# Kernel optimization log

Measured on AMD Instinct MI355X. Metric: run time of the kernel, lower is better.

Reference implementation:

```python
import jax, jax.numpy as jnp
import numpy as np

H = 256; NL = 6; N = 64; DCONV = 4; DIN = 512; HEADS = 8; P = 64
CONVD = DIN + 2 * N            # 640
PROJ = 2 * DIN + 2 * N + HEADS  # 1160


def rmsnorm(x, w, eps=1e-6):
    return x * jax.lax.rsqrt(jnp.mean(x * x, axis=-1, keepdims=True) + eps) * w


def mamba2(x, Win, conv_w, conv_b, dt_bias, A_log, D, gnorm, Wout):
    # x: (b, l, H)
    b, l, _ = x.shape
    zxbcdt = x @ Win                       # (b, l, PROJ)
    z = zxbcdt[..., :DIN]
    xBC = zxbcdt[..., DIN:DIN + CONVD]
    dt = zxbcdt[..., DIN + CONVD:]         # (b, l, HEADS)
    # causal depthwise conv1d along l
    xp = jnp.pad(xBC, ((0, 0), (DCONV - 1, 0), (0, 0)))
    xc = conv_b + sum(xp[:, k:k + l, :] * conv_w[k] for k in range(DCONV))
    xBC = jax.nn.silu(xc)
    xs = xBC[..., :DIN]
    B = xBC[..., DIN:DIN + N]
    C = xBC[..., DIN + N:]
    dt = jax.nn.softplus(dt + dt_bias)
    dA = jnp.exp(dt * (-jnp.exp(A_log)))   # (b, l, HEADS)
    xh = xs.reshape(b, l, HEADS, P)
    xdt = xh * dt[..., None]

    def step(h, inp):
        dA_t, xdt_t, B_t, C_t = inp
        h = dA_t[:, :, None, None] * h + xdt_t[..., None] * B_t[:, None, None, :]
        return h, jnp.einsum('bhpn,bn->bhp', h, C_t)

    h0 = jnp.zeros((b, HEADS, P, N), x.dtype)
    _, ys = jax.lax.scan(step, h0, (jnp.swapaxes(dA, 0, 1), jnp.swapaxes(xdt, 0, 1),
                                    jnp.swapaxes(B, 0, 1), jnp.swapaxes(C, 0, 1)))
    y = jnp.swapaxes(ys, 0, 1) + D[None, None, :, None] * xh   # (b, l, HEADS, P)
    y = y.reshape(b, l, DIN) * jax.nn.silu(z)
    return rmsnorm(y, gnorm) @ Wout


def dual_path(x, t_norm, t_Win, t_cw, t_cb, t_dtb, t_Alog, t_D, t_gn, t_Wout,
              b_norm, b_Win, b_cw, b_cb, b_dtb, b_Alog, b_D, b_gn, b_Wout):
    batch, time, bands, hdim = x.shape
    for i in range(NL):
        # time-axis pass (raw row-major reshape, matching torch .reshape semantics)
        xt = x.reshape(batch * bands, time, hdim)
        xt = xt + mamba2(rmsnorm(xt, t_norm[i]), t_Win[i], t_cw[i], t_cb[i],
                         t_dtb[i], t_Alog[i], t_D[i], t_gn[i], t_Wout[i])
        x = jnp.swapaxes(xt.reshape(batch, bands, time, hdim), 1, 2)
        # band-axis pass
        xb = x.reshape(batch * time, bands, hdim)
        xb = xb + mamba2(rmsnorm(xb, b_norm[i]), b_Win[i], b_cw[i], b_cb[i],
                         b_dtb[i], b_Alog[i], b_D[i], b_gn[i], b_Wout[i])
        x = xb.reshape(batch, time, bands, hdim)
    return x


def setup_inputs() -> dict:
    key = jax.random.key(0)
    ks = jax.random.split(key, 3)
    x = jax.random.normal(ks[0], (2, 512, 64, H), jnp.float32)

    def make_params(k):
        kk = jax.random.split(k, 5)
        g = lambda kx, sh, s: jax.random.normal(kx, sh, jnp.float32) * s
        return dict(
            norm=jnp.ones((NL, H), jnp.float32),
            Win=g(kk[0], (NL, H, PROJ), H ** -0.5),
            cw=g(kk[1], (NL, DCONV, CONVD), 0.2),
            cb=jnp.zeros((NL, CONVD), jnp.float32),
            dtb=g(kk[2], (NL, HEADS), 0.5),
            Alog=jnp.log(jnp.abs(g(kk[3], (NL, HEADS), 1.0)) + 0.5),
            D=jnp.ones((NL, HEADS), jnp.float32),
            gn=jnp.ones((NL, DIN), jnp.float32),
            Wout=g(kk[4], (NL, DIN, H), DIN ** -0.5),
        )

    tp = make_params(ks[1]); bp = make_params(ks[2])
    out = {'x': x}
    for name, d in (('t', tp), ('b', bp)):
        for kname, v in d.items():
            out[f'{name}_{kname}'] = v
    return out


def reference(x, t_norm, t_Win, t_cw, t_cb, t_dtb, t_Alog, t_D, t_gn, t_Wout,
              b_norm, b_Win, b_cw, b_cb, b_dtb, b_Alog, b_D, b_gn, b_Wout):
    return dual_path(x, t_norm, t_Win, t_cw, t_cb, t_dtb, t_Alog, t_D, t_gn, t_Wout,
                     b_norm, b_Win, b_cw, b_cb, b_dtb, b_Alog, b_D, b_gn, b_Wout)
```

## Files before the change

kernel.cpp:

```cpp
#include <hip/hip_runtime.h>
#include <math.h>

#define NLAY   6
#define Hd     256
#define DINv   512
#define NHEADS 8
#define CONVDv 640
#define PROJv  1160
#define ZW     656
#define NTOK   65536
#define NCH    1024

typedef __attribute__((ext_vector_type(8))) short bf16x8;
typedef __attribute__((ext_vector_type(4))) float f32x4;
typedef unsigned short u16;

__device__ __forceinline__ float siluf(float v) {
    return v * __builtin_amdgcn_rcpf(1.0f + __expf(-v));
}
__device__ __forceinline__ float bflo(unsigned u) { return __uint_as_float(u << 16); }
__device__ __forceinline__ float bfhi(unsigned u) { return __uint_as_float(u & 0xffff0000u); }
__device__ __forceinline__ u16 f2b(float f) {
    unsigned u = __float_as_uint(f);
    return (u16)((u + 0x7fffu + ((u >> 16) & 1u)) >> 16);
}
__device__ __forceinline__ float b2f(u16 s) { return __uint_as_float(((unsigned)s) << 16); }

__device__ __forceinline__ void gl_lds16(const void* g, void* l) {
    __builtin_amdgcn_global_load_lds((const __attribute__((address_space(1))) unsigned int*)g,
                                     (__attribute__((address_space(3))) unsigned int*)l, 16, 0, 0);
}

__global__ __launch_bounds__(512)
void kprep_win(const float* __restrict__ tW, const float* __restrict__ bW,
               u16* __restrict__ Whi, u16* __restrict__ Wlo)
{
    const int li = blockIdx.y, j = blockIdx.x;
    const int t  = threadIdx.x;
    const int kk = t >> 6, col = (t >> 2) & 15, quad = t & 3;
    const float* W = (li < 6) ? (tW + (size_t)li * Hd * PROJv)
                              : (bW + (size_t)(li - 6) * Hd * PROJv);
    const int fullcol = 16 * j + col;
    const size_t ob = ((size_t)li * 74 + j) * 4096 + kk * 512 + quad * 128 + col * 8;
#pragma unroll
    for (int e = 0; e < 8; e++) {
        const int k = kk * 32 + quad * 8 + e;
        const float v = (fullcol < PROJv) ? W[(size_t)k * PROJv + fullcol] : 0.f;
        const u16 hi = f2b(v);
        Whi[ob + e] = hi;
        Wlo[ob + e] = f2b(v - b2f(hi));
    }
}

__global__ __launch_bounds__(512)
void kprep_wout(const float* __restrict__ tW, const float* __restrict__ tg,
                const float* __restrict__ bW, const float* __restrict__ bg,
                u16* __restrict__ Whi, u16* __restrict__ Wlo)
{
    const int li = blockIdx.y, j = blockIdx.x;
    const int t  = threadIdx.x;
    const int kk = t >> 5, col = (t >> 1) & 15, qh = t & 1;
    const float* W = (li < 6) ? tW + (size_t)li * DINv * Hd : bW + (size_t)(li - 6) * DINv * Hd;
    const float* g = (li < 6) ? tg + li * DINv : bg + (li - 6) * DINv;
    const int fullcol = 16 * j + col;
#pragma unroll
    for (int q = 0; q < 2; q++) {
        const int quad = qh * 2 + q;
        const size_t ob = ((size_t)li * 16 + j) * 8192 + kk * 512 + quad * 128 + col * 8;
#pragma unroll
        for (int e = 0; e < 8; e++) {
            const int k = kk * 32 + quad * 8 + e;
            const float v = W[(size_t)k * Hd + fullcol] * g[k];
            const u16 hi = f2b(v);
            Whi[ob + e] = hi;
            Wlo[ob + e] = f2b(v - b2f(hi));
        }
    }
}

__global__ __launch_bounds__(512, 4)
void k1_mfma(const float* __restrict__ src, u16* __restrict__ zs,
             u16* __restrict__ xrawT, u16* __restrict__ bnd,
             const float* __restrict__ nw,
             const u16* __restrict__ Whi, const u16* __restrict__ Wlo)
{
    __shared__ __align__(16) char smem[67584];
    u16* sAh = (u16*)smem;
    u16* sAl = sAh + 64 * 264;
    const int tid = threadIdx.x;
    const int cb  = blockIdx.x;
    const int R0  = cb * 64;

    {
        const int tok = tid >> 3, l8 = tid & 7;
        const float* xr = src + ((size_t)(R0 + tok)) * Hd + l8 * 32;
        float vv[32];
#pragma unroll
        for (int q = 0; q < 8; q++) {
            float4 v = ((const float4*)xr)[q];
            vv[4*q] = v.x; vv[4*q+1] = v.y; vv[4*q+2] = v.z; vv[4*q+3] = v.w;
        }
        float ss = 0.f;
#pragma unroll
        for (int j = 0; j < 32; j++) ss += vv[j] * vv[j];
#pragma unroll
        for (int m = 4; m >= 1; m >>= 1) ss += __shfl_xor(ss, m, 8);
        const float rstd = rsqrtf(ss * (1.0f / Hd) + 1e-6f);
        const float* nr = nw + l8 * 32;
        u16* dh = sAh + tok * 264 + l8 * 32;
        u16* dl = sAl + tok * 264 + l8 * 32;
#pragma unroll
        for (int j = 0; j < 32; j++) {
            const float val = vv[j] * rstd * nr[j];
            const u16 hi = f2b(val);
            dh[j] = hi;
            dl[j] = f2b(val - b2f(hi));
        }
    }
    __syncthreads();

    const int lane = tid & 63, wave = tid >> 6;
    const int rh = wave >> 1, cw = wave & 1;
    const int quad = lane >> 4, m16 = lane & 15;

    bf16x8 ah[8], al[8];
    {
        const u16* ph = sAh + (rh * 16 + m16) * 264 + quad * 8;
        const u16* pl = sAl + (rh * 16 + m16) * 264 + quad * 8;
#pragma unroll
        for (int kk = 0; kk < 8; kk++) {
            ah[kk] = *(const bf16x8*)(ph + kk * 32);
            al[kk] = *(const bf16x8*)(pl + kk * 32);
        }
    }
    __syncthreads();

    u16* sW = (u16*)smem;

#define K1_STAGE(p, buf)                                                          \
    {                                                                             \
        const int obase = wave * 4096;                                            \
        _Pragma("unroll")                                                         \
        for (int i = 0; i < 4; i++) {                                             \
            const int o = obase + i * 1024;                                       \
            const int chunk = o >> 13, t2 = chunk >> 1, hl = chunk & 1;           \
            const int within = o & 8191;                                          \
            const u16* sbase = (hl ? Wlo : Whi) + (size_t)(2 * (p) + t2) * 4096;  \
            gl_lds16((const char*)sbase + within + lane * 16,                     \
                     (char*)sW + (buf) * 32768 + o);                              \
        }                                                                         \
    }

    K1_STAGE(0, 0);
    __syncthreads();

    for (int p = 0; p < 37; p++) {
        if (p < 36) K1_STAGE(p + 1, (p + 1) & 1);
        const int j = 2 * p + cw;
        const u16* tb = sW + (p & 1) * 16384 + cw * 8192 + lane * 8;
        f32x4 acc = (f32x4){0.f, 0.f, 0.f, 0.f};
#pragma unroll
        for (int kk = 0; kk < 8; kk++) {
            bf16x8 bh = *(const bf16x8*)(tb + kk * 512);
            bf16x8 bl = *(const bf16x8*)(tb + 4096 + kk * 512);
            acc = __builtin_amdgcn_mfma_f32_16x16x32_bf16(ah[kk], bh, acc, 0, 0, 0);
            acc = __builtin_amdgcn_mfma_f32_16x16x32_bf16(al[kk], bh, acc, 0, 0, 0);
            acc = __builtin_amdgcn_mfma_f32_16x16x32_bf16(ah[kk], bl, acc, 0, 0, 0);
        }
        const int fullcol = 16 * j + m16;
        if (j < 32) {
            u16* zr = zs + (size_t)(R0 + rh * 16 + quad * 4) * ZW + fullcol;
#pragma unroll
            for (int i = 0; i < 4; i++) zr[(size_t)i * ZW] = f2b(acc[i]);
        } else if (j < 64) {
            const int ch = fullcol - 512;
            uint2 v;
            v.x = (unsigned)f2b(acc[0]) | ((unsigned)f2b(acc[1]) << 16);
            v.y = (unsigned)f2b(acc[2]) | ((unsigned)f2b(acc[3]) << 16);
            *(uint2*)(xrawT + ((size_t)cb * 512 + ch) * 64 + rh * 16 + quad * 4) = v;
            if (rh == 3 && quad == 3) {
#pragma unroll
                for (int i = 1; i < 4; i++)
                    bnd[((size_t)cb * 3 + (i - 1)) * 640 + ch] = f2b(acc[i]);
            }
        } else if (j < 73) {
            const int zc = fullcol - 512;
            u16* zr = zs + (size_t)(R0 + rh * 16 + quad * 4) * ZW + zc;
#pragma unroll
            for (int i = 0; i < 4; i++) zr[(size_t)i * ZW] = f2b(acc[i]);
            if (j < 72 && rh == 3 && quad == 3) {
#pragma unroll
                for (int i = 1; i < 4; i++)
                    bnd[((size_t)cb * 3 + (i - 1)) * 640 + zc] = f2b(acc[i]);
            }
        }
        __syncthreads();
    }
#undef K1_STAGE
}

__device__ __forceinline__ void conv32_rmw(u16* xp, float w0, float w1, float w2, float w3,
                                           float bias, float h3, float h2, float h1)
{
    uint4 va = ((const uint4*)xp)[0], vb = ((const uint4*)xp)[1],
          vc = ((const uint4*)xp)[2], vd = ((const uint4*)xp)[3];
    unsigned uu[16] = {va.x, va.y, va.z, va.w, vb.x, vb.y, vb.z, vb.w,
                       vc.x, vc.y, vc.z, vc.w, vd.x, vd.y, vd.z, vd.w};
    unsigned ou[16];
#pragma unroll
    for (int k = 0; k < 16; k++) {
        const float x0 = bflo(uu[k]);
        const u16 o0 = f2b(siluf(bias + w0*h3 + w1*h2 + w2*h1 + w3*x0));
        h3 = h2; h2 = h1; h1 = x0;
        const float x1 = bfhi(uu[k]);
        const u16 o1 = f2b(siluf(bias + w0*h3 + w1*h2 + w2*h1 + w3*x1));
        h3 = h2; h2 = h1; h1 = x1;
        ou[k] = (unsigned)o0 | ((unsigned)o1 << 16);
    }
    ((uint4*)xp)[0] = make_uint4(ou[0],  ou[1],  ou[2],  ou[3]);
    ((uint4*)xp)[1] = make_uint4(ou[4],  ou[5],  ou[6],  ou[7]);
    ((uint4*)xp)[2] = make_uint4(ou[8],  ou[9],  ou[10], ou[11]);
    ((uint4*)xp)[3] = make_uint4(ou[12], ou[13], ou[14], ou[15]);
}

__global__ __launch_bounds__(256, 4)
void k2a_conv(u16* __restrict__ zs, u16* __restrict__ xrawT,
              float* __restrict__ spb, const u16* __restrict__ bnd,
              const float* __restrict__ cwp, const float* __restrict__ cbp,
              const float* __restrict__ dtbp, const float* __restrict__ alogp, int L)
{
    __shared__ __align__(16) u16 sBC[64][128];
    const int tid = threadIdx.x;
    const int cb  = blockIdx.x;
    const size_t row0 = (size_t)cb * 64;
    const bool atStart = (((int)(row0 % (size_t)L)) == 0);
    const int lane = tid & 63, wave = tid >> 6;

#pragma unroll
    for (int j = 0; j < 4; j++) {
        const int t0 = wave * 16 + j * 4;
        gl_lds16(zs + (row0 + t0 + (lane >> 4)) * ZW + 512 + (lane & 15) * 8,
                 (char*)sBC + t0 * 256);
    }

#pragma unroll
    for (int cc = 0; cc < 2; cc++) {
        const int ch = tid + cc * 256;
        const float w0 = cwp[0*CONVDv + ch], w1 = cwp[1*CONVDv + ch],
                    w2 = cwp[2*CONVDv + ch], w3 = cwp[3*CONVDv + ch];
        u16* xp = xrawT + ((size_t)cb * 512 + ch) * 64 + 32;
        const uint2 hv = *(const uint2*)(xp - 4);
        conv32_rmw(xp, w0, w1, w2, w3, cbp[ch], bfhi(hv.x), bflo(hv.y), bfhi(hv.y));
    }

    if (tid < 64) {
        const int t = tid;
        const uint4 dv = *(const uint4*)(zs + (row0 + t) * ZW + 640);
        const unsigned uu[4] = {dv.x, dv.y, dv.z, dv.w};
        float sp[8], ld[8];
#pragma unroll
        for (int h = 0; h < 8; h++) {
            const float d = ((h & 1) ? bfhi(uu[h >> 1]) : bflo(uu[h >> 1])) + dtbp[h];
            const float s = (d > 20.f) ? d : __logf(1.f + __expf(d));
            sp[h] = s;
            ld[h] = -__expf(alogp[h]) * s;
        }
        float* ob = spb + (row0 + t) * 24;
        *(float4*)(ob)      = make_float4(sp[0], sp[1], sp[2], sp[3]);
        *(float4*)(ob + 4)  = make_float4(sp[4], sp[5], sp[6], sp[7]);
        *(float4*)(ob + 8)  = make_float4(ld[0], ld[1], ld[2], ld[3]);
        *(float4*)(ob + 12) = make_float4(ld[4], ld[5], ld[6], ld[7]);
    }
    __syncthreads();

#pragma unroll
    for (int cc = 0; cc < 2; cc++) {
        const int ch = tid + cc * 256;
        const float w0 = cwp[0*CONVDv + ch], w1 = cwp[1*CONVDv + ch],
                    w2 = cwp[2*CONVDv + ch], w3 = cwp[3*CONVDv + ch];
        float h1 = 0.f, h2 = 0.f, h3 = 0.f;
        if (!atStart) {
            const u16* bp = bnd + ((size_t)(cb - 1) * 3) * 640 + ch;
            h3 = b2f(bp[0]); h2 = b2f(bp[640]); h1 = b2f(bp[1280]);
        }
        conv32_rmw(xrawT + ((size_t)cb * 512 + ch) * 64, w0, w1, w2, w3, cbp[ch], h3, h2, h1);
    }

    u16 o[32];
    {
        const int ch  = tid & 127;
        const int th  = tid >> 7;
        const int t0  = th * 32;
        const int gch = 512 + ch;
        const float w0 = cwp[0*CONVDv + gch], w1 = cwp[1*CONVDv + gch],
                    w2 = cwp[2*CONVDv + gch], w3 = cwp[3*CONVDv + gch];
        const float bias = cbp[gch];
        float h1, h2, h3;
        if (th) {
            h3 = b2f(sBC[29][ch]); h2 = b2f(sBC[30][ch]); h1 = b2f(sBC[31][ch]);
        } else if (!atStart) {
            const u16* bp = bnd + ((size_t)(cb - 1) * 3) * 640 + gch;
            h3 = b2f(bp[0]); h2 = b2f(bp[640]); h1 = b2f(bp[1280]);
        } else { h1 = h2 = h3 = 0.f; }
#pragma unroll
        for (int t = 0; t < 32; t++) {
            const float xv = b2f(sBC[t0 + t][ch]);
            o[t] = f2b(siluf(bias + w0*h3 + w1*h2 + w2*h1 + w3*xv));
            h3 = h2; h2 = h1; h1 = xv;
        }
    }
    __syncthreads();
    {
        const int ch = tid & 127, t0 = (tid >> 7) * 32;
#pragma unroll
        for (int t = 0; t < 32; t++) sBC[t0 + t][ch] = o[t];
    }
    __syncthreads();
#pragma unroll
    for (int i = 0; i < 4; i++) {
        const int g = tid + i * 256;
        const int t = g >> 4, s16 = g & 15;
        *(uint4*)(zs + (row0 + t) * ZW + 512 + s16 * 8) = *(const uint4*)(&sBC[t][s16 * 8]);
    }
}

template<bool TMODE>
__global__ __launch_bounds__(256, 3)
void k2b_ssd(u16* __restrict__ zs, u16* __restrict__ xrawT,
             float* __restrict__ spb, u16* __restrict__ Sbuf,
             const float* __restrict__ Dp)
{
    __shared__ __align__(16) float sG[64][68];
    __shared__ float sClog[NHEADS][64];
    __shared__ float sSp[NHEADS][64];
    __shared__ float sWd[NHEADS][64];
    __shared__ __align__(16) u16 sBT[64][72];
    const int tid = threadIdx.x;
    const int lane = tid & 63, wave = tid >> 6;
    const int quad = lane >> 4, m16 = lane & 15;
    const int cb = blockIdx.x;
    const size_t row0 = (size_t)cb * 64;

    if (TMODE) {
        const int t_ = tid >> 2, ns = (tid & 3) * 16;
        const u16* br = zs + (row0 + t_) * ZW + 512 + ns;
        uint4 a = ((const uint4*)br)[0], b = ((const uint4*)br)[1];
        unsigned uu[8] = {a.x, a.y, a.z, a.w, b.x, b.y, b.z, b.w};
#pragma unroll
        for (int k = 0; k < 8; k++) {
            sBT[ns + 2*k][t_]     = (u16)(uu[k] & 0xffff);
            sBT[ns + 2*k + 1][t_] = (u16)(uu[k] >> 16);
        }
    }

    {
        const u16* cp = zs + (row0 + 16 * wave + m16) * ZW + 576 + quad * 8;
        bf16x8 cf0 = *(const bf16x8*)(cp);
        bf16x8 cf1 = *(const bf16x8*)(cp + 32);
#pragma unroll
        for (int st = 0; st < 4; st++) {
            const u16* bp = zs + (row0 + 16 * st + m16) * ZW + 512 + quad * 8;
            f32x4 acc = (f32x4){0.f, 0.f, 0.f, 0.f};
            acc = __builtin_amdgcn_mfma_f32_16x16x32_bf16(cf0, *(const bf16x8*)(bp), acc, 0, 0, 0);
            acc = __builtin_amdgcn_mfma_f32_16x16x32_bf16(cf1, *(const bf16x8*)(bp + 32), acc, 0, 0, 0);
#pragma unroll
            for (int i = 0; i < 4; i++)
                sG[16 * wave + quad * 4 + i][16 * st + m16] = acc[i];
        }
    }

#pragma unroll
    for (int hh = 0; hh < 2; hh++) {
        const int h = wave * 2 + hh;
        float c = spb[(row0 + lane) * 24 + 8 + h];
        const float sp = spb[(row0 + lane) * 24 + h];
#pragma unroll
        for (int d = 1; d < 64; d <<= 1) {
            const float o = __shfl_up(c, d, 64);
            if (lane >= d) c += o;
        }
        sClog[h][lane] = c;
        sSp[h][lane] = sp;
        if (TMODE) {
            spb[(row0 + lane) * 24 + 16 + h] = __expf(c);
            const float cl63 = __shfl(c, 63, 64);
            sWd[h][lane] = __expf(cl63 - c) * sp;
        }
    }
    __syncthreads();

    if (TMODE) {
        for (int h = 0; h < NHEADS; h++) {
            bf16x8 Ahi[2], Alo[2];
#pragma unroll
            for (int kk = 0; kk < 2; kk++) {
                const u16* xp = xrawT + ((size_t)cb * 512 + h * 64 + 16 * wave + m16) * 64
                                + 32 * kk + quad * 8;
                bf16x8 xf = *(const bf16x8*)xp;
                const float* wp = &sWd[h][32 * kk + quad * 8];
#pragma unroll
                for (int j = 0; j < 8; j++) {
                    const float v = b2f((u16)xf[j]) * wp[j];
                    const u16 hi = f2b(v);
                    Ahi[kk][j] = (short)hi;
                    Alo[kk][j] = (short)f2b(v - b2f(hi));
                }
            }
            u16* sb = Sbuf + ((size_t)cb * 8 + h) * 4096;
#pragma unroll
            for (int nt = 0; nt < 4; nt++) {
                f32x4 acc = (f32x4){0.f, 0.f, 0.f, 0.f};
#pragma unroll
                for (int kk = 0; kk < 2; kk++) {
                    const bf16x8 bf_ = *(const bf16x8*)(&sBT[16 * nt + m16][32 * kk + quad * 8]);
                    acc = __builtin_amdgcn_mfma_f32_16x16x32_bf16(Ahi[kk], bf_, acc, 0, 0, 0);
                    acc = __builtin_amdgcn_mfma_f32_16x16x32_bf16(Alo[kk], bf_, acc, 0, 0, 0);
                }
#pragma unroll
                for (int i = 0; i < 4; i++)
                    sb[(16 * wave + quad * 4 + i) * 64 + 16 * nt + m16] = f2b(acc[i]);
            }
        }
        __syncthreads();
    }

    const int t = 16 * wave + m16;
    for (int h = 0; h < NHEADS; h++) {
        const float Dh = Dp[h];
        const float clt = sClog[h][t];
        bf16x8 Mhi[2], Mlo[2];
#pragma unroll
        for (int kk = 0; kk < 2; kk++) {
            const float* gp = &sG[t][32 * kk + quad * 8];
            const float* cp = &sClog[h][32 * kk + quad * 8];
            const float* pp = &sSp[h][32 * kk + quad * 8];
#pragma unroll
            for (int j = 0; j < 8; j++) {
                const int s = 32 * kk + quad * 8 + j;
                float m = (s <= t) ? (__expf(clt - cp[j]) * pp[j] * gp[j]) : 0.f;
                if (s == t) m += Dh;
                const u16 hi = f2b(m);
                Mhi[kk][j] = (short)hi;
                Mlo[kk][j] = (short)f2b(m - b2f(hi));
            }
        }
        bf16x8 xf[4][2];
#pragma unroll
        for (int pt = 0; pt < 4; pt++)
#pragma unroll
            for (int kk = 0; kk < 2; kk++)
                xf[pt][kk] = *(const bf16x8*)(xrawT
                    + ((size_t)cb * 512 + h * 64 + 16 * pt + m16) * 64 + 32 * kk + quad * 8);
        if (TMODE) __syncthreads();
        f32x4 accY[4];
#pragma unroll
        for (int pt = 0; pt < 4; pt++) {
            accY[pt] = (f32x4){0.f, 0.f, 0.f, 0.f};
#pragma unroll
            for (int kk = 0; kk < 2; kk++) {
                accY[pt] = __builtin_amdgcn_mfma_f32_16x16x32_bf16(Mhi[kk], xf[pt][kk], accY[pt], 0, 0, 0);
                accY[pt] = __builtin_amdgcn_mfma_f32_16x16x32_bf16(Mlo[kk], xf[pt][kk], accY[pt], 0, 0, 0);
            }
        }
#pragma unroll
        for (int pt = 0; pt < 4; pt++) {
            if (TMODE) {
                uint2 v;
                v.x = (unsigned)f2b(accY[pt][0]) | ((unsigned)f2b(accY[pt][1]) << 16);
                v.y = (unsigned)f2b(accY[pt][2]) | ((unsigned)f2b(accY[pt][3]) << 16);
                *(uint2*)(xrawT + ((size_t)cb * 512 + h * 64 + 16 * pt + m16) * 64
                          + 16 * wave + quad * 4) = v;
            } else {
#pragma unroll
                for (int i = 0; i < 4; i++) {
                    const size_t row = row0 + 16 * wave + quad * 4 + i;
                    const int col = h * 64 + 16 * pt + m16;
                    const u16 zv = zs[row * ZW + col];
                    zs[row * ZW + col] = f2b(accY[pt][i] * siluf(b2f(zv)));
                }
            }
        }
    }
}

__global__ __launch_bounds__(64, 4)
void k2c_states(u16* __restrict__ Sbuf, const float* __restrict__ spb)
{
    const int p = threadIdx.x, h = blockIdx.y, s = blockIdx.x;
    float H[64];
#pragma unroll
    for (int n = 0; n < 64; n++) H[n] = 0.f;
    for (int c = 1; c < 8; c++) {
        const float P = spb[((size_t)s * 512 + (c - 1) * 64 + 63) * 24 + 16 + h];
        u16* sp_ = Sbuf + (((size_t)(s * 8 + c - 1) * 8 + h) * 4096) + p * 64;
#pragma unroll
        for (int n = 0; n < 64; n += 8) {
            uint4 v = *(const uint4*)(sp_ + n);
            unsigned uu[4] = {v.x, v.y, v.z, v.w};
            float sv[8];
#pragma unroll
            for (int w2 = 0; w2 < 4; w2++) { sv[2*w2] = bflo(uu[w2]); sv[2*w2+1] = bfhi(uu[w2]); }
#pragma unroll
            for (int e = 0; e < 8; e++) H[n + e] = fmaf(P, H[n + e], sv[e]);
            uint4 o;
            o.x = (unsigned)f2b(H[n+0]) | ((unsigned)f2b(H[n+1]) << 16);
            o.y = (unsigned)f2b(H[n+2]) | ((unsigned)f2b(H[n+3]) << 16);
            o.z = (unsigned)f2b(H[n+4]) | ((unsigned)f2b(H[n+5]) << 16);
            o.w = (unsigned)f2b(H[n+6]) | ((unsigned)f2b(H[n+7]) << 16);
            *(uint4*)(sp_ + n) = o;
        }
    }
}

__global__ __launch_bounds__(256, 4)
void k2d_corr(u16* __restrict__ zs, const u16* __restrict__ xrawT,
              const float* __restrict__ spb, const u16* __restrict__ Sbuf)
{
    const int tid = threadIdx.x;
    const int lane = tid & 63, wave = tid >> 6;
    const int quad = lane >> 4, m16 = lane & 15;
    const int cb = blockIdx.x;
    const int c = cb & 7;
    const size_t row0 = (size_t)cb * 64;

    for (int h = 0; h < NHEADS; h++) {
        f32x4 acc[4];
#pragma unroll
        for (int pt = 0; pt < 4; pt++) {
            const uint2 v = *(const uint2*)(xrawT
                + ((size_t)cb * 512 + h * 64 + 16 * pt + m16) * 64 + 16 * wave + quad * 4);
            acc[pt][0] = bflo(v.x); acc[pt][1] = bfhi(v.x);
            acc[pt][2] = bflo(v.y); acc[pt][3] = bfhi(v.y);
        }
        if (c) {
            const float at = spb[(row0 + 16 * wave + m16) * 24 + 16 + h];
            bf16x8 Ahi[2], Alo[2];
#pragma unroll
            for (int kk = 0; kk < 2; kk++) {
                const u16* cp = zs + (row0 + 16 * wave + m16) * ZW + 576 + 32 * kk + quad * 8;
                bf16x8 cf = *(const bf16x8*)cp;
#pragma unroll
                for (int j = 0; j < 8; j++) {
                    const float v = b2f((u16)cf[j]) * at;
                    const u16 hi = f2b(v);
                    Ahi[kk][j] = (short)hi;
                    Alo[kk][j] = (short)f2b(v - b2f(hi));
                }
            }
            const u16* hb = Sbuf + ((size_t)(cb - 1) * 8 + h) * 4096;
#pragma unroll
            for (int pt = 0; pt < 4; pt++) {
#pragma unroll
                for (int kk = 0; kk < 2; kk++) {
                    bf16x8 hf = *(const bf16x8*)(hb + (16 * pt + m16) * 64 + 32 * kk + quad * 8);
                    acc[pt] = __builtin_amdgcn_mfma_f32_16x16x32_bf16(Ahi[kk], hf, acc[pt], 0, 0, 0);
                    acc[pt] = __builtin_amdgcn_mfma_f32_16x16x32_bf16(Alo[kk], hf, acc[pt], 0, 0, 0);
                }
            }
        }
#pragma unroll
        for (int pt = 0; pt < 4; pt++) {
#pragma unroll
            for (int i = 0; i < 4; i++) {
                const size_t row = row0 + 16 * wave + quad * 4 + i;
                const int col = h * 64 + 16 * pt + m16;
                const u16 zv = zs[row * ZW + col];
                zs[row * ZW + col] = f2b(acc[pt][i] * siluf(b2f(zv)));
            }
        }
    }
}

template<bool TMODE>
__global__ __launch_bounds__(512, 2)
void k3_mfma(const u16* __restrict__ zs, const float* __restrict__ src,
             float* __restrict__ dst,
             const u16* __restrict__ Whi, const u16* __restrict__ Wlo)
{
    __shared__ __align__(16) char smem[66560];
    float* sAf = (float*)smem;
    const int tid = threadIdx.x;
    const int R0  = blockIdx.x * 128;
    const int lane = tid & 63, wave = tid >> 6;
    const int quad = lane >> 4, m16 = lane & 15;

    bf16x8 ah[16], al[16];

    for (int b = 0; b < 4; b++) {
        {
            const int tok = tid >> 4, l16 = tid & 15;
            const u16* yr = zs + (size_t)(R0 + b * 32 + tok) * ZW + l16 * 32;
            float v[32];
#pragma unroll
            for (int q = 0; q < 4; q++) {
                uint4 u = ((const uint4*)yr)[q];
                unsigned uu[4] = {u.x, u.y, u.z, u.w};
#pragma unroll
                for (int w2 = 0; w2 < 4; w2++) {
                    v[8*q + 2*w2]     = bflo(uu[w2]);
                    v[8*q + 2*w2 + 1] = bfhi(uu[w2]);
                }
            }
            float ss = 0.f;
#pragma unroll
            for (int j = 0; j < 32; j++) ss += v[j] * v[j];
#pragma unroll
            for (int m = 8; m >= 1; m >>= 1) ss += __shfl_xor(ss, m, 16);
            const float rstd = rsqrtf(ss * (1.0f / DINv) + 1e-6f);
            float* dp = sAf + tok * 516 + l16 * 32;
#pragma unroll
            for (int j = 0; j < 32; j++) dp[j] = v[j] * rstd;
        }
        __syncthreads();
        if ((wave >> 1) == b) {
            const int r = (wave & 1) * 16 + m16;
            const float* fp = sAf + r * 516 + quad * 8;
#pragma unroll
            for (int kk = 0; kk < 16; kk++) {
                float4 fa = ((const float4*)(fp + kk * 32))[0];
                float4 fb = ((const float4*)(fp + kk * 32))[1];
                float f[8] = {fa.x, fa.y, fa.z, fa.w, fb.x, fb.y, fb.z, fb.w};
                bf16x8 hv, lv;
#pragma unroll
                for (int e = 0; e < 8; e++) {
                    const u16 hi = f2b(f[e]);
                    hv[e] = (short)hi;
                    lv[e] = (short)f2b(f[e] - b2f(hi));
                }
                ah[kk] = hv;
                al[kk] = lv;
            }
        }
        __syncthreads();
    }

    f32x4 acc[16];
#pragma unroll
    for (int j = 0; j < 16; j++) acc[j] = (f32x4){0.f, 0.f, 0.f, 0.f};

#define K3_STAGE(j, buf)                                                          \
    {                                                                             \
        const int obase = wave * 4096;                                            \
        _Pragma("unroll")                                                         \
        for (int i = 0; i < 4; i++) {                                             \
            const int o = obase + i * 1024;                                       \
            const char* gsrc = (o < 16384)                                        \
                ? ((const char*)(Whi + (size_t)(j) * 8192) + o)                   \
                : ((const char*)(Wlo + (size_t)(j) * 8192) + (o - 16384));        \
            gl_lds16(gsrc + lane * 16, smem + (buf) * 32768 + o);                 \
        }                                                                         \
    }

    K3_STAGE(0, 0);
    __syncthreads();

    for (int j = 0; j < 16; j++) {
        if (j < 15) K3_STAGE(j + 1, (j + 1) & 1);
        const u16* tb = (const u16*)(smem + (j & 1) * 32768) + lane * 8;
#pragma unroll
        for (int kk = 0; kk < 16; kk++) {
            bf16x8 bh = *(const bf16x8*)(tb + kk * 512);
            bf16x8 bl = *(const bf16x8*)(tb + 8192 + kk * 512);
            acc[j] = __builtin_amdgcn_mfma_f32_16x16x32_bf16(ah[kk], bh, acc[j], 0, 0, 0);
            acc[j] = __builtin_amdgcn_mfma_f32_16x16x32_bf16(al[kk], bh, acc[j], 0, 0, 0);
            acc[j] = __builtin_amdgcn_mfma_f32_16x16x32_bf16(ah[kk], bl, acc[j], 0, 0, 0);
        }
        __syncthreads();
    }
#undef K3_STAGE

#pragma unroll
    for (int j = 0; j < 16; j++) {
        const int col = 16 * j + m16;
#pragma unroll
        for (int i = 0; i < 4; i++) {
            const size_t inrow = (size_t)(R0 + wave * 16 + quad * 4 + i);
            const float v = acc[j][i] + src[inrow * Hd + col];
            size_t orow;
            if (TMODE) {
                const size_t sq = inrow >> 9;
                const size_t tt = inrow & 511;
                orow = ((sq >> 6) * 512 + tt) * 64 + (sq & 63);
            } else {
                orow = inrow;
            }
            dst[orow * Hd + col] = v;
        }
    }
}

extern "C" void kernel_launch(void* const* d_in, const int* in_sizes, int n_in,
                              void* d_out, int out_size, void* d_ws, size_t ws_size,
                              hipStream_t stream) {
    const float* x      = (const float*)d_in[0];
    const float* t_norm = (const float*)d_in[1];
    const float* t_Win  = (const float*)d_in[2];
    const float* t_cw   = (const float*)d_in[3];
    const float* t_cb   = (const float*)d_in[4];
    const float* t_dtb  = (const float*)d_in[5];
    const float* t_Alog = (const float*)d_in[6];
    const float* t_D    = (const float*)d_in[7];
    const float* t_gn   = (const float*)d_in[8];
    const float* t_Wout = (const float*)d_in[9];
    const float* b_norm = (const float*)d_in[10];
    const float* b_Win  = (const float*)d_in[11];
    const float* b_cw   = (const float*)d_in[12];
    const float* b_cb   = (const float*)d_in[13];
    const float* b_dtb  = (const float*)d_in[14];
    const float* b_Alog = (const float*)d_in[15];
    const float* b_D    = (const float*)d_in[16];
    const float* b_gn   = (const float*)d_in[17];
    const float* b_Wout = (const float*)d_in[18];

    float* out = (float*)d_out;
    char*  wsb = (char*)d_ws;
    float* xbuf = (float*)wsb;
    u16*   Sbuf = (u16*)wsb;
    size_t off = 67108864;
    u16* W1hi = (u16*)(wsb + off); off += (size_t)12 * 74 * 4096 * 2;
    u16* W1lo = (u16*)(wsb + off); off += (size_t)12 * 74 * 4096 * 2;
    u16* W2hi = (u16*)(wsb + off); off += (size_t)12 * 16 * 8192 * 2;
    u16* W2lo = (u16*)(wsb + off); off += (size_t)12 * 16 * 8192 * 2;
    u16* zs   = (u16*)(wsb + off); off += (size_t)NTOK * ZW * 2;
    float* spb = (float*)(wsb + off); off += (size_t)NTOK * 24 * 4;
    u16* xrawT = (u16*)(wsb + off); off += (size_t)NTOK * 512 * 2;
    u16* bnd  = (u16*)(wsb + off);

    kprep_win<<<dim3(74, 12), 512, 0, stream>>>(t_Win, b_Win, W1hi, W1lo);
    kprep_wout<<<dim3(16, 12), 512, 0, stream>>>(t_Wout, t_gn, b_Wout, b_gn, W2hi, W2lo);

    for (int i = 0; i < NLAY; i++) {
        const float* src_t = (i == 0) ? x : out;
        k1_mfma<<<NCH, 512, 0, stream>>>(src_t, zs, xrawT, bnd, t_norm + i * Hd,
                 W1hi + (size_t)i * 74 * 4096, W1lo + (size_t)i * 74 * 4096);
        k2a_conv<<<NCH, 256, 0, stream>>>(zs, xrawT, spb, bnd,
                 t_cw + i * 4 * CONVDv, t_cb + i * CONVDv, t_dtb + i * NHEADS,
                 t_Alog + i * NHEADS, 512);
        k2b_ssd<true><<<NCH, 256, 0, stream>>>(zs, xrawT, spb, Sbuf, t_D + i * NHEADS);
        k2c_states<<<dim3(128, NHEADS), 64, 0, stream>>>(Sbuf, spb);
        k2d_corr<<<NCH, 256, 0, stream>>>(zs, xrawT, spb, Sbuf);
        k3_mfma<true><<<NTOK/128, 512, 0, stream>>>(zs, src_t, xbuf,
                 W2hi + (size_t)i * 16 * 8192, W2lo + (size_t)i * 16 * 8192);
        k1_mfma<<<NCH, 512, 0, stream>>>(xbuf, zs, xrawT, bnd, b_norm + i * Hd,
                 W1hi + (size_t)(i + 6) * 74 * 4096, W1lo + (size_t)(i + 6) * 74 * 4096);
        k2a_conv<<<NCH, 256, 0, stream>>>(zs, xrawT, spb, bnd,
                 b_cw + i * 4 * CONVDv, b_cb + i * CONVDv, b_dtb + i * NHEADS,
                 b_Alog + i * NHEADS, 64);
        k2b_ssd<false><<<NCH, 256, 0, stream>>>(zs, xrawT, spb, Sbuf, b_D + i * NHEADS);
        k3_mfma<false><<<NTOK/128, 512, 0, stream>>>(zs, xbuf, out,
                 W2hi + (size_t)(i + 6) * 16 * 8192, W2lo + (size_t)(i + 6) * 16 * 8192);
    }
}
```

Before: 5.837 ms.

## Restructure output projection: smaller blocks, register RMSnorm, streamed accumulators

```diff
diff --git a/kernel.cpp b/kernel.cpp
--- a/kernel.cpp
+++ b/kernel.cpp
@@ -572,121 +572,101 @@
 }
 
 template<bool TMODE>
-__global__ __launch_bounds__(512, 2)
+__global__ __launch_bounds__(256, 3)
 void k3_mfma(const u16* __restrict__ zs, const float* __restrict__ src,
              float* __restrict__ dst,
              const u16* __restrict__ Whi, const u16* __restrict__ Wlo)
 {
-    __shared__ __align__(16) char smem[66560];
-    float* sAf = (float*)smem;
+    __shared__ __align__(16) char smem[32768];
     const int tid = threadIdx.x;
-    const int R0  = blockIdx.x * 128;
+    const int cb  = blockIdx.x;
+    const int R0  = cb * 64;
     const int lane = tid & 63, wave = tid >> 6;
     const int quad = lane >> 4, m16 = lane & 15;
 
+#define K3_STAGE(hc)                                                              \
+    {                                                                             \
+        const int jj = (hc) >> 1;                                                 \
+        const char* wb = (const char*)((((hc) & 1) ? Wlo : Whi) + (size_t)jj * 8192); \
+        char* db = smem + ((hc) & 1) * 16384 + wave * 4096;                       \
+        _Pragma("unroll")                                                         \
+        for (int i = 0; i < 4; i++)                                               \
+            gl_lds16(wb + wave * 4096 + i * 1024 + lane * 16, db + i * 1024);     \
+    }
+
+    K3_STAGE(0);
+
+    const u16* yr = zs + (size_t)(R0 + wave * 16 + m16) * ZW + quad * 8;
+    float ss = 0.f;
+#pragma unroll
+    for (int kk = 0; kk < 16; kk++) {
+        uint4 u = *(const uint4*)(yr + kk * 32);
+        unsigned uu[4] = {u.x, u.y, u.z, u.w};
+#pragma unroll
+        for (int w2 = 0; w2 < 4; w2++) {
+            const float a = bflo(uu[w2]), b = bfhi(uu[w2]);
+            ss += a * a + b * b;
+        }
+    }
+    ss += __shfl_xor(ss, 16, 64);
+    ss += __shfl_xor(ss, 32, 64);
+    const float rstd = rsqrtf(ss * (1.0f / DINv) + 1e-6f);
+
     bf16x8 ah[16], al[16];
-
-    for (int b = 0; b < 4; b++) {
+#pragma unroll
+    for (int kk = 0; kk < 16; kk++) {
+        uint4 u = *(const uint4*)(yr + kk * 32);
+        unsigned uu[4] = {u.x, u.y, u.z, u.w};
+#pragma unroll
+        for (int w2 = 0; w2 < 4; w2++) {
+            const float a = bflo(uu[w2]) * rstd;
+            const float b = bfhi(uu[w2]) * rstd;
+            u16 hi = f2b(a);
+            ah[kk][2*w2]   = (short)hi; al[kk][2*w2]   = (short)f2b(a - b2f(hi));
+            hi = f2b(b);
+            ah[kk][2*w2+1] = (short)hi; al[kk][2*w2+1] = (short)f2b(b - b2f(hi));
+        }
+    }
+    __syncthreads();
+
+    for (int j = 0; j < 16; j++) {
+        K3_STAGE(2 * j + 1);
+        f32x4 acc = (f32x4){0.f, 0.f, 0.f, 0.f};
+        const u16* tb0 = (const u16*)smem + lane * 8;
+#pragma unroll
+        for (int kk = 0; kk < 16; kk++) {
+            bf16x8 bh = *(const bf16x8*)(tb0 + kk * 512);
+            acc = __builtin_amdgcn_mfma_f32_16x16x32_bf16(ah[kk], bh, acc, 0, 0, 0);
+            acc = __builtin_amdgcn_mfma_f32_16x16x32_bf16(al[kk], bh, acc, 0, 0, 0);
+        }
+        __syncthreads();
+        if (j < 15) K3_STAGE(2 * j + 2);
+        const u16* tb1 = (const u16*)(smem + 16384) + lane * 8;
+#pragma unroll
+        for (int kk = 0; kk < 16; kk++) {
+            bf16x8 bl = *(const bf16x8*)(tb1 + kk * 512);
+            acc = __builtin_amdgcn_mfma_f32_16x16x32_bf16(ah[kk], bl, acc, 0, 0, 0);
+        }
         {
-            const int tok = tid >> 4, l16 = tid & 15;
-            const u16* yr = zs + (size_t)(R0 + b * 32 + tok) * ZW + l16 * 32;
-            float v[32];
-#pragma unroll
-            for (int q = 0; q < 4; q++) {
-                uint4 u = ((const uint4*)yr)[q];
-                unsigned uu[4] = {u.x, u.y, u.z, u.w};
-#pragma unroll
-                for (int w2 = 0; w2 < 4; w2++) {
-                    v[8*q + 2*w2]     = bflo(uu[w2]);
-                    v[8*q + 2*w2 + 1] = bfhi(uu[w2]);
+            const int col = 16 * j + m16;
+#pragma unroll
+            for (int i = 0; i < 4; i++) {
+                const size_t inrow = (size_t)(R0 + wave * 16 + quad * 4 + i);
+                const float v = acc[i] + src[inrow * Hd + col];
+                size_t orow;
+                if (TMODE) {
+                    const size_t sq = inrow >> 9;
+                    const size_t tt = inrow & 511;
+                    orow = ((sq >> 6) * 512 + tt) * 64 + (sq & 63);
+                } else {
+                    orow = inrow;
                 }
-            }
-            float ss = 0.f;
-#pragma unroll
-            for (int j = 0; j < 32; j++) ss += v[j] * v[j];
-#pragma unroll
-            for (int m = 8; m >= 1; m >>= 1) ss += __shfl_xor(ss, m, 16);
-            const float rstd = rsqrtf(ss * (1.0f / DINv) + 1e-6f);
-            float* dp = sAf + tok * 516 + l16 * 32;
-#pragma unroll
-            for (int j = 0; j < 32; j++) dp[j] = v[j] * rstd;
+                dst[orow * Hd + col] = v;
+            }
         }
         __syncthreads();
-        if ((wave >> 1) == b) {
-            const int r = (wave & 1) * 16 + m16;
-            const float* fp = sAf + r * 516 + quad * 8;
-#pragma unroll
-            for (int kk = 0; kk < 16; kk++) {
-                float4 fa = ((const float4*)(fp + kk * 32))[0];
-                float4 fb = ((const float4*)(fp + kk * 32))[1];
-                float f[8] = {fa.x, fa.y, fa.z, fa.w, fb.x, fb.y, fb.z, fb.w};
-                bf16x8 hv, lv;
-#pragma unroll
-                for (int e = 0; e < 8; e++) {
-                    const u16 hi = f2b(f[e]);
-                    hv[e] = (short)hi;
-                    lv[e] = (short)f2b(f[e] - b2f(hi));
-                }
-                ah[kk] = hv;
-                al[kk] = lv;
-            }
-        }
-        __syncthreads();
-    }
-
-    f32x4 acc[16];
-#pragma unroll
-    for (int j = 0; j < 16; j++) acc[j] = (f32x4){0.f, 0.f, 0.f, 0.f};
-
-#define K3_STAGE(j, buf)                                                          \
-    {                                                                             \
-        const int obase = wave * 4096;                                            \
-        _Pragma("unroll")                                                         \
-        for (int i = 0; i < 4; i++) {                                             \
-            const int o = obase + i * 1024;                                       \
-            const char* gsrc = (o < 16384)                                        \
-                ? ((const char*)(Whi + (size_t)(j) * 8192) + o)                   \
-                : ((const char*)(Wlo + (size_t)(j) * 8192) + (o - 16384));        \
-            gl_lds16(gsrc + lane * 16, smem + (buf) * 32768 + o);                 \
-        }                                                                         \
-    }
-
-    K3_STAGE(0, 0);
-    __syncthreads();
-
-    for (int j = 0; j < 16; j++) {
-        if (j < 15) K3_STAGE(j + 1, (j + 1) & 1);
-        const u16* tb = (const u16*)(smem + (j & 1) * 32768) + lane * 8;
-#pragma unroll
-        for (int kk = 0; kk < 16; kk++) {
-            bf16x8 bh = *(const bf16x8*)(tb + kk * 512);
-            bf16x8 bl = *(const bf16x8*)(tb + 8192 + kk * 512);
-            acc[j] = __builtin_amdgcn_mfma_f32_16x16x32_bf16(ah[kk], bh, acc[j], 0, 0, 0);
-            acc[j] = __builtin_amdgcn_mfma_f32_16x16x32_bf16(al[kk], bh, acc[j], 0, 0, 0);
-            acc[j] = __builtin_amdgcn_mfma_f32_16x16x32_bf16(ah[kk], bl, acc[j], 0, 0, 0);
-        }
-        __syncthreads();
     }
 #undef K3_STAGE
-
-#pragma unroll
-    for (int j = 0; j < 16; j++) {
-        const int col = 16 * j + m16;
-#pragma unroll
-        for (int i = 0; i < 4; i++) {
-            const size_t inrow = (size_t)(R0 + wave * 16 + quad * 4 + i);
-            const float v = acc[j][i] + src[inrow * Hd + col];
-            size_t orow;
-            if (TMODE) {
-                const size_t sq = inrow >> 9;
-                const size_t tt = inrow & 511;
-                orow = ((sq >> 6) * 512 + tt) * 64 + (sq & 63);
-            } else {
-                orow = inrow;
-            }
-            dst[orow * Hd + col] = v;
-        }
-    }
 }
 
 extern "C" void kernel_launch(void* const* d_in, const int* in_sizes, int n_in,
@@ -739,7 +719,7 @@
         k2b_ssd<true><<<NCH, 256, 0, stream>>>(zs, xrawT, spb, Sbuf, t_D + i * NHEADS);
         k2c_states<<<dim3(128, NHEADS), 64, 0, stream>>>(Sbuf, spb);
         k2d_corr<<<NCH, 256, 0, stream>>>(zs, xrawT, spb, Sbuf);
-        k3_mfma<true><<<NTOK/128, 512, 0, stream>>>(zs, src_t, xbuf,
+        k3_mfma<true><<<NCH, 256, 0, stream>>>(zs, src_t, xbuf,
                  W2hi + (size_t)i * 16 * 8192, W2lo + (size_t)i * 16 * 8192);
         k1_mfma<<<NCH, 512, 0, stream>>>(xbuf, zs, xrawT, bnd, b_norm + i * Hd,
                  W1hi + (size_t)(i + 6) * 74 * 4096, W1lo + (size_t)(i + 6) * 74 * 4096);
@@ -747,7 +727,7 @@
                  b_cw + i * 4 * CONVDv, b_cb + i * CONVDv, b_dtb + i * NHEADS,
                  b_Alog + i * NHEADS, 64);
         k2b_ssd<false><<<NCH, 256, 0, stream>>>(zs, xrawT, spb, Sbuf, b_D + i * NHEADS);
-        k3_mfma<false><<<NTOK/128, 512, 0, stream>>>(zs, xbuf, out,
+        k3_mfma<false><<<NCH, 256, 0, stream>>>(zs, xbuf, out,
                  W2hi + (size_t)(i + 6) * 16 * 8192, W2lo + (size_t)(i + 6) * 16 * 8192);
     }
 }
```

New measurement: 6.315 ms. 8.2% more time.
